# Optimization experiments

Measured on AMD Instinct MI355X. Metric: run time of the kernel, lower is better.

The kernel has to match this reference:

```python
import jax, jax.numpy as jnp
import numpy as np

SMOOTH = 1e-5  # MONAI DiceLoss smooth_nr / smooth_dr defaults
BETA = 1.0


def setup_inputs() -> dict:
    key = jax.random.key(0)
    k1, k2, k3 = jax.random.split(key, 3)
    B, C, H, W = 8, 16, 512, 512
    outputs = jax.random.normal(k1, (B, C, H, W), dtype=jnp.float32)
    targets = jax.random.randint(k2, (B, 1, H, W), 0, C, dtype=jnp.int64)
    matrix_penalty = jax.random.uniform(k3, (C, C), dtype=jnp.float32)
    return {
        "outputs": outputs,
        "targets": targets,
        "matrix_penalty": matrix_penalty,
        "N_classes": C,
        "Npixels": H * W,
        "length_targets": B,
        "total_batch": B,
    }


def _domino_loss(outputs, matrix_penalty, t, N_classes, total_batch):
    # outputs: [B, C, H, W] logits; t: [B, H, W] int labels
    logp = jax.nn.log_softmax(outputs, axis=1)          # [B, C, H, W]
    probs = jnp.exp(logp)
    probs_bhwc = jnp.moveaxis(probs, 1, -1)             # [B, H, W, C]
    onehot = jax.nn.one_hot(t, N_classes, dtype=outputs.dtype)  # [B, H, W, C]

    # Cross-entropy term (mean over all pixels), as in CrossEntropyLoss
    ce = -jnp.mean(jnp.sum(onehot * jnp.moveaxis(logp, 1, -1), axis=-1))

    # Dice term (softmax probs vs one-hot target, per batch x class, mean)
    inter = jnp.sum(probs_bhwc * onehot, axis=(1, 2))   # [B, C]
    denom = jnp.sum(probs_bhwc, axis=(1, 2)) + jnp.sum(onehot, axis=(1, 2))
    dice = jnp.mean(1.0 - (2.0 * inter + SMOOTH) / (denom + SMOOTH))

    # DOMINO penalty: per pixel, one_hot(target)^T @ matrix_penalty @ softmax(logits)
    # = matrix_penalty[target] . probs  (gather row instead of tiny matmul)
    pen_rows = matrix_penalty[t]                        # [B, H, W, C]
    penalty = jnp.sum(pen_rows * probs_bhwc)

    return ce + dice + BETA * penalty / total_batch


def reference(outputs, targets, matrix_penalty, N_classes, Npixels, length_targets, total_batch):
    t = targets[:, 0].astype(jnp.int32)                 # [B, H, W]
    return _domino_loss(outputs, matrix_penalty, t, N_classes, total_batch)
```

## Files before the change

### kernel.cpp

```cpp
#include <hip/hip_runtime.h>

#define NC      16
#define HW      (512 * 512)
#define NB      8
#define BPB     128
#define NBLK    (NB * BPB)
#define THREADS 256
#define PXR     256
#define ROUNDS  8
#define SMOOTH  1e-5f

__global__ __launch_bounds__(THREADS) void domino_main(
    const float* __restrict__ logits,
    const int*   __restrict__ tgt,
    const float* __restrict__ penalty,
    float*       __restrict__ P)
{
    __shared__ float bufA[NC * PXR];
    __shared__ float bufB[NC * PXR];
    __shared__ float pen_t[NC * NC];
    __shared__ float red[4][34];

    const int tid = threadIdx.x;
    const int b   = blockIdx.x / BPB;
    const int blk = blockIdx.x % BPB;

    if (tid < NC * NC) {
        const int r = tid / NC, c = tid % NC;
        pen_t[c * NC + r] = penalty[tid];
    }

    const float* ob   = logits + (size_t)b * NC * HW;
    const int*   tb   = tgt    + (size_t)b * HW;
    const int    base = blk * (ROUNDS * PXR);

#pragma unroll
    for (int j = 0; j < 4; ++j) {
        const int i = j * THREADS + tid;
        const int c = i >> 6, f = i & 63;
        const float4 v = *(const float4*)(ob + (size_t)c * HW + base + f * 4);
        *(float4*)&bufA[c * PXR + f * 4] = v;
    }
    int tcur = tb[base + tid];

    float inter_acc[NC], denom_acc[NC];
#pragma unroll
    for (int c = 0; c < NC; ++c) { inter_acc[c] = 0.f; denom_acc[c] = 0.f; }
    float ce_acc = 0.f, pen_acc = 0.f;

    __syncthreads();

#pragma unroll 2
    for (int r = 0; r < ROUNDS; ++r) {
        float* const curb = (r & 1) ? bufB : bufA;
        float* const nxtb = (r & 1) ? bufA : bufB;

        float4 g0, g1, g2, g3;
        int tn = 0;
        if (r + 1 < ROUNDS) {
            const int pix1 = base + (r + 1) * PXR;
            { const int i = 0 * THREADS + tid, c = i >> 6, f = i & 63;
              g0 = *(const float4*)(ob + (size_t)c * HW + pix1 + f * 4); }
            { const int i = 1 * THREADS + tid, c = i >> 6, f = i & 63;
              g1 = *(const float4*)(ob + (size_t)c * HW + pix1 + f * 4); }
            { const int i = 2 * THREADS + tid, c = i >> 6, f = i & 63;
              g2 = *(const float4*)(ob + (size_t)c * HW + pix1 + f * 4); }
            { const int i = 3 * THREADS + tid, c = i >> 6, f = i & 63;
              g3 = *(const float4*)(ob + (size_t)c * HW + pix1 + f * 4); }
            tn = tb[pix1 + tid];
        }

        {
            const int t = tcur;
            float e[NC], s = 0.f;
#pragma unroll
            for (int c = 0; c < NC; ++c) {
                e[c] = __expf(curb[c * PXR + tid]);
                s += e[c];
            }
            float et = 0.f;
#pragma unroll
            for (int c = 0; c < NC; ++c) et = (t == c) ? e[c] : et;
            const float inv = 1.0f / s;
            ce_acc -= __logf(et * inv);
            float pdot = 0.f;
#pragma unroll
            for (int c = 0; c < NC; ++c) {
                const float p = e[c] * inv;
                denom_acc[c] += p + ((t == c) ? 1.f : 0.f);
                inter_acc[c] += (t == c) ? p : 0.f;
                pdot += pen_t[c * NC + t] * p;
            }
            pen_acc += pdot;
        }

        if (r + 1 < ROUNDS) {
            { const int i = 0 * THREADS + tid, c = i >> 6, f = i & 63;
              *(float4*)&nxtb[c * PXR + f * 4] = g0; }
            { const int i = 1 * THREADS + tid, c = i >> 6, f = i & 63;
              *(float4*)&nxtb[c * PXR + f * 4] = g1; }
            { const int i = 2 * THREADS + tid, c = i >> 6, f = i & 63;
              *(float4*)&nxtb[c * PXR + f * 4] = g2; }
            { const int i = 3 * THREADS + tid, c = i >> 6, f = i & 63;
              *(float4*)&nxtb[c * PXR + f * 4] = g3; }
            tcur = tn;
        }
        __syncthreads();
    }

#pragma unroll
    for (int c = 0; c < NC; ++c) {
#pragma unroll
        for (int off = 32; off; off >>= 1) {
            inter_acc[c] += __shfl_xor(inter_acc[c], off);
            denom_acc[c] += __shfl_xor(denom_acc[c], off);
        }
    }
#pragma unroll
    for (int off = 32; off; off >>= 1) {
        ce_acc  += __shfl_xor(ce_acc,  off);
        pen_acc += __shfl_xor(pen_acc, off);
    }

    const int lane = tid & 63, wid = tid >> 6;
    if (lane == 0) {
#pragma unroll
        for (int c = 0; c < NC; ++c) {
            red[wid][c]      = inter_acc[c];
            red[wid][NC + c] = denom_acc[c];
        }
        red[wid][32] = ce_acc;
        red[wid][33] = pen_acc;
    }
    __syncthreads();

    if (tid < 34) {
        const float v = red[0][tid] + red[1][tid] + red[2][tid] + red[3][tid];
        P[tid * NBLK + blockIdx.x] = v;
    }
}

__global__ __launch_bounds__(1024) void domino_final(
    const float* __restrict__ P, float* __restrict__ out)
{
    __shared__ float dice_l[128], ce_l[16], pen_l[16];

    const int tid = threadIdx.x;
    const int bin = tid >> 3, j = tid & 7;
    const int c = bin >> 3, b = bin & 7;

    const float4* ip = (const float4*)(P + (size_t)c        * NBLK + b * BPB) + j * 4;
    const float4* dp = (const float4*)(P + (size_t)(NC + c) * NBLK + b * BPB) + j * 4;
    float inter = 0.f, denom = 0.f;
#pragma unroll
    for (int k = 0; k < 4; ++k) {
        const float4 a = ip[k]; inter += a.x + a.y + a.z + a.w;
        const float4 d = dp[k]; denom += d.x + d.y + d.z + d.w;
    }
#pragma unroll
    for (int off = 4; off; off >>= 1) {
        inter += __shfl_xor(inter, off);
        denom += __shfl_xor(denom, off);
    }
    if (j == 0)
        dice_l[bin] = 1.0f - (2.0f * inter + SMOOTH) / (denom + SMOOTH);

    float ce  = P[32 * NBLK + tid];
    float pen = P[33 * NBLK + tid];
#pragma unroll
    for (int off = 32; off; off >>= 1) {
        ce  += __shfl_xor(ce,  off);
        pen += __shfl_xor(pen, off);
    }
    const int lane = tid & 63, wid = tid >> 6;
    if (lane == 0) { ce_l[wid] = ce; pen_l[wid] = pen; }
    __syncthreads();

    if (tid < 64) {
        float d = dice_l[tid] + dice_l[tid + 64];
#pragma unroll
        for (int off = 32; off; off >>= 1) d += __shfl_xor(d, off);
        if (tid == 0) {
            float ces = 0.f, pens = 0.f;
#pragma unroll
            for (int i = 0; i < 16; ++i) { ces += ce_l[i]; pens += pen_l[i]; }
            out[0] = ces  * (1.0f / (8.0f * 262144.0f))
                   + d    * (1.0f / 128.0f)
                   + pens * (1.0f / 8.0f);
        }
    }
}

extern "C" void kernel_launch(void* const* d_in, const int* in_sizes, int n_in,
                              void* d_out, int out_size, void* d_ws, size_t ws_size,
                              hipStream_t stream)
{
    const float* logits = (const float*)d_in[0];
    const int*   tgt    = (const int*)d_in[1];
    const float* pen    = (const float*)d_in[2];
    float*       P      = (float*)d_ws;
    float*       out    = (float*)d_out;

    domino_main<<<NBLK, THREADS, 0, stream>>>(logits, tgt, pen, P);
    domino_final<<<1, 1024, 0, stream>>>(P, out);
}
```

Before: 40.68 us.

## Use 1024-thread blocks with one wave per class channel and fewer blocks

Grows the main kernel to 1024 threads and 1024-pixel rounds, cutting the grid to 256 blocks. Each wave now loads one class channel, so every wave reads one contiguous region. The final reduction is resized to 256 threads to match the smaller partial array. The aim is fewer block-level partial reductions and more coalesced loads per wave. In exchange, shared memory per block grows to 128 KB, which allows roughly one block per CU, and the 256 blocks may not fill all CUs on the GPU.

```diff
diff --git a/kernel.cpp b/kernel.cpp
--- a/kernel.cpp
+++ b/kernel.cpp
@@ -3,10 +3,10 @@
 #define NC      16
 #define HW      (512 * 512)
 #define NB      8
-#define BPB     128
+#define BPB     32
 #define NBLK    (NB * BPB)
-#define THREADS 256
-#define PXR     256
+#define THREADS 1024
+#define PXR     1024
 #define ROUNDS  8
 #define SMOOTH  1e-5f
 
@@ -19,11 +19,13 @@
     __shared__ float bufA[NC * PXR];
     __shared__ float bufB[NC * PXR];
     __shared__ float pen_t[NC * NC];
-    __shared__ float red[4][34];
-
-    const int tid = threadIdx.x;
-    const int b   = blockIdx.x / BPB;
-    const int blk = blockIdx.x % BPB;
+    __shared__ float red[16][34];
+
+    const int tid  = threadIdx.x;
+    const int w    = tid >> 6;
+    const int lane = tid & 63;
+    const int b    = blockIdx.x / BPB;
+    const int blk  = blockIdx.x % BPB;
 
     if (tid < NC * NC) {
         const int r = tid / NC, c = tid % NC;
@@ -32,14 +34,18 @@
 
     const float* ob   = logits + (size_t)b * NC * HW;
     const int*   tb   = tgt    + (size_t)b * HW;
+    const float* cls  = ob + (size_t)w * HW;
     const int    base = blk * (ROUNDS * PXR);
 
-#pragma unroll
-    for (int j = 0; j < 4; ++j) {
-        const int i = j * THREADS + tid;
-        const int c = i >> 6, f = i & 63;
-        const float4 v = *(const float4*)(ob + (size_t)c * HW + base + f * 4);
-        *(float4*)&bufA[c * PXR + f * 4] = v;
+    {
+        const float4 a0 = *(const float4*)(cls + base +   0 + lane * 4);
+        const float4 a1 = *(const float4*)(cls + base + 256 + lane * 4);
+        const float4 a2 = *(const float4*)(cls + base + 512 + lane * 4);
+        const float4 a3 = *(const float4*)(cls + base + 768 + lane * 4);
+        *(float4*)&bufA[w * PXR +   0 + lane * 4] = a0;
+        *(float4*)&bufA[w * PXR + 256 + lane * 4] = a1;
+        *(float4*)&bufA[w * PXR + 512 + lane * 4] = a2;
+        *(float4*)&bufA[w * PXR + 768 + lane * 4] = a3;
     }
     int tcur = tb[base + tid];
 
@@ -50,7 +56,6 @@
 
     __syncthreads();
 
-#pragma unroll 2
     for (int r = 0; r < ROUNDS; ++r) {
         float* const curb = (r & 1) ? bufB : bufA;
         float* const nxtb = (r & 1) ? bufA : bufB;
@@ -58,16 +63,12 @@
         float4 g0, g1, g2, g3;
         int tn = 0;
         if (r + 1 < ROUNDS) {
-            const int pix1 = base + (r + 1) * PXR;
-            { const int i = 0 * THREADS + tid, c = i >> 6, f = i & 63;
-              g0 = *(const float4*)(ob + (size_t)c * HW + pix1 + f * 4); }
-            { const int i = 1 * THREADS + tid, c = i >> 6, f = i & 63;
-              g1 = *(const float4*)(ob + (size_t)c * HW + pix1 + f * 4); }
-            { const int i = 2 * THREADS + tid, c = i >> 6, f = i & 63;
-              g2 = *(const float4*)(ob + (size_t)c * HW + pix1 + f * 4); }
-            { const int i = 3 * THREADS + tid, c = i >> 6, f = i & 63;
-              g3 = *(const float4*)(ob + (size_t)c * HW + pix1 + f * 4); }
-            tn = tb[pix1 + tid];
+            const int p1 = base + (r + 1) * PXR;
+            g0 = *(const float4*)(cls + p1 +   0 + lane * 4);
+            g1 = *(const float4*)(cls + p1 + 256 + lane * 4);
+            g2 = *(const float4*)(cls + p1 + 512 + lane * 4);
+            g3 = *(const float4*)(cls + p1 + 768 + lane * 4);
+            tn = tb[p1 + tid];
         }
 
         {
@@ -95,14 +96,10 @@
         }
 
         if (r + 1 < ROUNDS) {
-            { const int i = 0 * THREADS + tid, c = i >> 6, f = i & 63;
-              *(float4*)&nxtb[c * PXR + f * 4] = g0; }
-            { const int i = 1 * THREADS + tid, c = i >> 6, f = i & 63;
-              *(float4*)&nxtb[c * PXR + f * 4] = g1; }
-            { const int i = 2 * THREADS + tid, c = i >> 6, f = i & 63;
-              *(float4*)&nxtb[c * PXR + f * 4] = g2; }
-            { const int i = 3 * THREADS + tid, c = i >> 6, f = i & 63;
-              *(float4*)&nxtb[c * PXR + f * 4] = g3; }
+            *(float4*)&nxtb[w * PXR +   0 + lane * 4] = g0;
+            *(float4*)&nxtb[w * PXR + 256 + lane * 4] = g1;
+            *(float4*)&nxtb[w * PXR + 512 + lane * 4] = g2;
+            *(float4*)&nxtb[w * PXR + 768 + lane * 4] = g3;
             tcur = tn;
         }
         __syncthreads();
@@ -122,46 +119,44 @@
         pen_acc += __shfl_xor(pen_acc, off);
     }
 
-    const int lane = tid & 63, wid = tid >> 6;
     if (lane == 0) {
 #pragma unroll
         for (int c = 0; c < NC; ++c) {
-            red[wid][c]      = inter_acc[c];
-            red[wid][NC + c] = denom_acc[c];
-        }
-        red[wid][32] = ce_acc;
-        red[wid][33] = pen_acc;
+            red[w][c]      = inter_acc[c];
+            red[w][NC + c] = denom_acc[c];
+        }
+        red[w][32] = ce_acc;
+        red[w][33] = pen_acc;
     }
     __syncthreads();
 
     if (tid < 34) {
-        const float v = red[0][tid] + red[1][tid] + red[2][tid] + red[3][tid];
+        float v = 0.f;
+#pragma unroll
+        for (int i = 0; i < 16; ++i) v += red[i][tid];
         P[tid * NBLK + blockIdx.x] = v;
     }
 }
 
-__global__ __launch_bounds__(1024) void domino_final(
+__global__ __launch_bounds__(256) void domino_final(
     const float* __restrict__ P, float* __restrict__ out)
 {
-    __shared__ float dice_l[128], ce_l[16], pen_l[16];
+    __shared__ float dice_l[128], ce_l[4], pen_l[4], dice_w[2];
 
     const int tid = threadIdx.x;
-    const int bin = tid >> 3, j = tid & 7;
-    const int c = bin >> 3, b = bin & 7;
-
-    const float4* ip = (const float4*)(P + (size_t)c        * NBLK + b * BPB) + j * 4;
-    const float4* dp = (const float4*)(P + (size_t)(NC + c) * NBLK + b * BPB) + j * 4;
+    const int bin = tid >> 1, j = tid & 1;
+    const int c = bin >> 3, bb = bin & 7;
+
+    const float* ip = P + (size_t)c        * NBLK + bb * BPB + j * 16;
+    const float* dp = P + (size_t)(NC + c) * NBLK + bb * BPB + j * 16;
     float inter = 0.f, denom = 0.f;
 #pragma unroll
     for (int k = 0; k < 4; ++k) {
-        const float4 a = ip[k]; inter += a.x + a.y + a.z + a.w;
-        const float4 d = dp[k]; denom += d.x + d.y + d.z + d.w;
-    }
-#pragma unroll
-    for (int off = 4; off; off >>= 1) {
-        inter += __shfl_xor(inter, off);
-        denom += __shfl_xor(denom, off);
-    }
+        const float4 a = *(const float4*)(ip + 4 * k); inter += a.x + a.y + a.z + a.w;
+        const float4 d = *(const float4*)(dp + 4 * k); denom += d.x + d.y + d.z + d.w;
+    }
+    inter += __shfl_xor(inter, 1);
+    denom += __shfl_xor(denom, 1);
     if (j == 0)
         dice_l[bin] = 1.0f - (2.0f * inter + SMOOTH) / (denom + SMOOTH);
 
@@ -176,18 +171,18 @@
     if (lane == 0) { ce_l[wid] = ce; pen_l[wid] = pen; }
     __syncthreads();
 
-    if (tid < 64) {
-        float d = dice_l[tid] + dice_l[tid + 64];
+    if (tid < 128) {
+        float d = dice_l[tid];
 #pragma unroll
         for (int off = 32; off; off >>= 1) d += __shfl_xor(d, off);
-        if (tid == 0) {
-            float ces = 0.f, pens = 0.f;
-#pragma unroll
-            for (int i = 0; i < 16; ++i) { ces += ce_l[i]; pens += pen_l[i]; }
-            out[0] = ces  * (1.0f / (8.0f * 262144.0f))
-                   + d    * (1.0f / 128.0f)
-                   + pens * (1.0f / 8.0f);
-        }
+        if ((tid & 63) == 0) dice_w[tid >> 6] = d;
+    }
+    __syncthreads();
+
+    if (tid == 0) {
+        out[0] = (ce_l[0] + ce_l[1] + ce_l[2] + ce_l[3]) * (1.0f / (8.0f * 262144.0f))
+               + (dice_w[0] + dice_w[1]) * (1.0f / 128.0f)
+               + (pen_l[0] + pen_l[1] + pen_l[2] + pen_l[3]) * (1.0f / 8.0f);
     }
 }
 
@@ -202,5 +197,5 @@
     float*       out    = (float*)d_out;
 
     domino_main<<<NBLK, THREADS, 0, stream>>>(logits, tgt, pen, P);
-    domino_final<<<1, 1024, 0, stream>>>(P, out);
+    domino_final<<<1, 256, 0, stream>>>(P, out);
 }
```

After: 38.90 us. -4.4%, faster.

## Stage logits and targets via direct global-to-LDS loads with triple buffering

Applied to the files above, without the earlier changes.

Replaces register-staged double buffering with __builtin_amdgcn_global_load_lds transfers straight into a three-slot LDS ring, issued two rounds ahead and waited on with explicit s_waitcnt vmcnt plus a raw s_barrier. Targets are also staged through LDS instead of per-thread register prefetch. The aim is to remove the VGPR round trip and LDS store instructions and to keep more loads in flight. It relies on hand-counted vmcnt values matching the five loads per round, and it uses more LDS per block, which may lower occupancy.

```diff
diff --git a/kernel.cpp b/kernel.cpp
--- a/kernel.cpp
+++ b/kernel.cpp
@@ -10,22 +10,36 @@
 #define ROUNDS  8
 #define SMOOTH  1e-5f
 
+typedef __attribute__((address_space(3))) unsigned int       lds_u32;
+typedef __attribute__((address_space(1))) const unsigned int glb_u32;
+
+__device__ __forceinline__ void stage16(const float* g, float* l) {
+    __builtin_amdgcn_global_load_lds((glb_u32*)(const void*)g,
+                                     (lds_u32*)(void*)l, 16, 0, 0);
+}
+__device__ __forceinline__ void stage4(const int* g, int* l) {
+    __builtin_amdgcn_global_load_lds((glb_u32*)(const void*)g,
+                                     (lds_u32*)(void*)l, 4, 0, 0);
+}
+
 __global__ __launch_bounds__(THREADS) void domino_main(
     const float* __restrict__ logits,
     const int*   __restrict__ tgt,
     const float* __restrict__ penalty,
     float*       __restrict__ P)
 {
-    __shared__ float bufA[NC * PXR];
-    __shared__ float bufB[NC * PXR];
+    __shared__ float buf[3][NC * PXR];
+    __shared__ int   tbuf[3][PXR];
     __shared__ float pen_t[NC * NC];
     __shared__ float red[4][34];
 
-    const int tid = threadIdx.x;
-    const int b   = blockIdx.x / BPB;
-    const int blk = blockIdx.x % BPB;
-
-    if (tid < NC * NC) {
+    const int tid  = threadIdx.x;
+    const int w    = tid >> 6;
+    const int lane = tid & 63;
+    const int b    = blockIdx.x / BPB;
+    const int blk  = blockIdx.x % BPB;
+
+    {
         const int r = tid / NC, c = tid % NC;
         pen_t[c * NC + r] = penalty[tid];
     }
@@ -34,48 +48,42 @@
     const int*   tb   = tgt    + (size_t)b * HW;
     const int    base = blk * (ROUNDS * PXR);
 
-#pragma unroll
-    for (int j = 0; j < 4; ++j) {
-        const int i = j * THREADS + tid;
-        const int c = i >> 6, f = i & 63;
-        const float4 v = *(const float4*)(ob + (size_t)c * HW + base + f * 4);
-        *(float4*)&bufA[c * PXR + f * 4] = v;
-    }
-    int tcur = tb[base + tid];
+#define ISSUE(RR, SLOT) do {                                                   \
+        const int off = base + (RR) * PXR;                                     \
+        float* const dst = &buf[(SLOT)][0];                                    \
+        stage16(ob + (size_t)(4*w+0) * HW + off + lane * 4, dst + (4*w+0) * PXR); \
+        stage16(ob + (size_t)(4*w+1) * HW + off + lane * 4, dst + (4*w+1) * PXR); \
+        stage16(ob + (size_t)(4*w+2) * HW + off + lane * 4, dst + (4*w+2) * PXR); \
+        stage16(ob + (size_t)(4*w+3) * HW + off + lane * 4, dst + (4*w+3) * PXR); \
+        stage4(tb + off + w * 64 + lane, &tbuf[(SLOT)][w * 64]);               \
+    } while (0)
+
+    ISSUE(0, 0);
+    ISSUE(1, 1);
 
     float inter_acc[NC], denom_acc[NC];
 #pragma unroll
     for (int c = 0; c < NC; ++c) { inter_acc[c] = 0.f; denom_acc[c] = 0.f; }
     float ce_acc = 0.f, pen_acc = 0.f;
 
-    __syncthreads();
-
-#pragma unroll 2
+#pragma unroll
     for (int r = 0; r < ROUNDS; ++r) {
-        float* const curb = (r & 1) ? bufB : bufA;
-        float* const nxtb = (r & 1) ? bufA : bufB;
-
-        float4 g0, g1, g2, g3;
-        int tn = 0;
-        if (r + 1 < ROUNDS) {
-            const int pix1 = base + (r + 1) * PXR;
-            { const int i = 0 * THREADS + tid, c = i >> 6, f = i & 63;
-              g0 = *(const float4*)(ob + (size_t)c * HW + pix1 + f * 4); }
-            { const int i = 1 * THREADS + tid, c = i >> 6, f = i & 63;
-              g1 = *(const float4*)(ob + (size_t)c * HW + pix1 + f * 4); }
-            { const int i = 2 * THREADS + tid, c = i >> 6, f = i & 63;
-              g2 = *(const float4*)(ob + (size_t)c * HW + pix1 + f * 4); }
-            { const int i = 3 * THREADS + tid, c = i >> 6, f = i & 63;
-              g3 = *(const float4*)(ob + (size_t)c * HW + pix1 + f * 4); }
-            tn = tb[pix1 + tid];
-        }
+        if (r < ROUNDS - 1)
+            asm volatile("s_waitcnt vmcnt(5) lgkmcnt(0)" ::: "memory");
+        else
+            asm volatile("s_waitcnt vmcnt(0) lgkmcnt(0)" ::: "memory");
+        __builtin_amdgcn_sched_barrier(0);
+        __builtin_amdgcn_s_barrier();
+        __builtin_amdgcn_sched_barrier(0);
+        if (r + 2 < ROUNDS) ISSUE(r + 2, (r + 2) % 3);
 
         {
-            const int t = tcur;
+            const float* const cb = &buf[r % 3][0];
+            const int t = tbuf[r % 3][tid];
             float e[NC], s = 0.f;
 #pragma unroll
             for (int c = 0; c < NC; ++c) {
-                e[c] = __expf(curb[c * PXR + tid]);
+                e[c] = __expf(cb[c * PXR + tid]);
                 s += e[c];
             }
             float et = 0.f;
@@ -93,20 +101,8 @@
             }
             pen_acc += pdot;
         }
-
-        if (r + 1 < ROUNDS) {
-            { const int i = 0 * THREADS + tid, c = i >> 6, f = i & 63;
-              *(float4*)&nxtb[c * PXR + f * 4] = g0; }
-            { const int i = 1 * THREADS + tid, c = i >> 6, f = i & 63;
-              *(float4*)&nxtb[c * PXR + f * 4] = g1; }
-            { const int i = 2 * THREADS + tid, c = i >> 6, f = i & 63;
-              *(float4*)&nxtb[c * PXR + f * 4] = g2; }
-            { const int i = 3 * THREADS + tid, c = i >> 6, f = i & 63;
-              *(float4*)&nxtb[c * PXR + f * 4] = g3; }
-            tcur = tn;
-        }
-        __syncthreads();
-    }
+    }
+#undef ISSUE
 
 #pragma unroll
     for (int c = 0; c < NC; ++c) {
@@ -122,15 +118,14 @@
         pen_acc += __shfl_xor(pen_acc, off);
     }
 
-    const int lane = tid & 63, wid = tid >> 6;
     if (lane == 0) {
 #pragma unroll
         for (int c = 0; c < NC; ++c) {
-            red[wid][c]      = inter_acc[c];
-            red[wid][NC + c] = denom_acc[c];
-        }
-        red[wid][32] = ce_acc;
-        red[wid][33] = pen_acc;
+            red[w][c]      = inter_acc[c];
+            red[w][NC + c] = denom_acc[c];
+        }
+        red[w][32] = ce_acc;
+        red[w][33] = pen_acc;
     }
     __syncthreads();
 
@@ -147,10 +142,10 @@
 
     const int tid = threadIdx.x;
     const int bin = tid >> 3, j = tid & 7;
-    const int c = bin >> 3, b = bin & 7;
-
-    const float4* ip = (const float4*)(P + (size_t)c        * NBLK + b * BPB) + j * 4;
-    const float4* dp = (const float4*)(P + (size_t)(NC + c) * NBLK + b * BPB) + j * 4;
+    const int c = bin >> 3, bb = bin & 7;
+
+    const float4* ip = (const float4*)(P + (size_t)c        * NBLK + bb * BPB) + j * 4;
+    const float4* dp = (const float4*)(P + (size_t)(NC + c) * NBLK + bb * BPB) + j * 4;
     float inter = 0.f, denom = 0.f;
 #pragma unroll
     for (int k = 0; k < 4; ++k) {
```

Result: slower. 43.75 us (+7.5%).
